# Optimization experiments

Hardware: AMD Instinct MI355X
Metric: run time of the kernel (lower is better)

Reference implementation:

```python
import jax, jax.numpy as jnp
import numpy as np

R = 128            # dense leaf-grid resolution (stand-in for N^3 octree leaves)
N_STEPS = 192      # fixed marching budget (replaces data-dependent while loop)
STEP_SIZE = 0.001
BACKGROUND = 1.0
DELTA_SCALE = 1.0  # 1/invradius with tree radius 1


def setup_inputs() -> dict:
    key = jax.random.key(0)
    k1, k2, k3, k4 = jax.random.split(key, 4)
    B = 65536
    grid = jax.random.normal(k1, (R, R, R, 4), dtype=jnp.float32)
    origins = jax.random.uniform(k2, (B, 3), dtype=jnp.float32)          # inside unit cube
    dirs = jax.random.normal(k3, (B, 3), dtype=jnp.float32)
    viewdirs = jax.random.normal(k4, (B, 3), dtype=jnp.float32)
    return {"grid": grid, "origins": origins, "dirs": dirs, "viewdirs": viewdirs}


def _dda_unit(cen, invdir):
    # entry/exit of ray cen + t*dir vs the unit cube [0,1]^3
    t1 = -cen * invdir            # [B,3]
    t2 = t1 + invdir
    lo = jnp.minimum(t1, t2)
    hi = jnp.maximum(t1, t2)
    tmin = jnp.maximum(jnp.max(lo, axis=-1), 0.0)   # [B]
    tmax = jnp.minimum(jnp.min(hi, axis=-1), 1e9)   # [B]
    return tmin, tmax


def _render(grid, origins, dirs, viewdirs):
    del viewdirs  # RGBA data_format: no SH basis evaluation
    dirs = dirs / jnp.linalg.norm(dirs, axis=-1, keepdims=True)
    invdirs = 1.0 / (dirs + 1e-9)
    t, tmax = _dda_unit(origins, invdirs)
    B = origins.shape[0]
    light = jnp.ones((B,), dtype=origins.dtype)
    out_rgb = jnp.zeros((B, 3), dtype=origins.dtype)
    cube_sz = 1.0 / R

    def step(carry, _):
        t, light, out_rgb = carry
        active = t < tmax
        pos = origins + t[:, None] * dirs                      # [B,3]
        idxf = jnp.floor(pos * R)
        idx = jnp.clip(idxf.astype(jnp.int32), 0, R - 1)       # voxel index
        rgba = grid[idx[:, 0], idx[:, 1], idx[:, 2]]           # [B,4] gather
        pos_t = pos * R - idx.astype(pos.dtype)                # local coords in voxel
        smin, smax = _dda_unit(pos_t, invdirs)
        delta_t = (smax - smin) * cube_sz + STEP_SIZE          # [B]
        sigma = jax.nn.relu(rgba[:, 3])
        att = jnp.exp(-delta_t * sigma * DELTA_SCALE)
        weight = light * (1.0 - att)
        rgb = jax.nn.sigmoid(rgba[:, :3])
        out_rgb = out_rgb + jnp.where(active[:, None], weight[:, None] * rgb, 0.0)
        light = jnp.where(active, light * att, light)
        t = jnp.where(active, t + delta_t, t)
        return (t, light, out_rgb), None

    (t, light, out_rgb), _ = jax.lax.scan(step, (t, light, out_rgb), None, length=N_STEPS)
    return out_rgb + BACKGROUND * light[:, None]


def reference(grid, origins, dirs, viewdirs):
    return _render(grid, origins, dirs, viewdirs)
```

## Files before the change

### kernel.cpp

```cpp
#include <hip/hip_runtime.h>


constexpr int   R_DIM    = 128;
constexpr int   N_VOX    = R_DIM * R_DIM * R_DIM;
constexpr int   N_STEPS  = 192;
constexpr int   NSEG     = 4;
constexpr int   SEG_LEN  = N_STEPS / NSEG;
constexpr float STEP_SZ  = 0.001f;
constexpr float CUBE_SZ  = 1.0f / 128.0f;
constexpr int   PIPE     = 8;
constexpr float SIG_MAX  = 5.5f;

__device__ __forceinline__ float sigmoid_fast(float x) {
    return __builtin_amdgcn_rcpf(1.0f + __expf(-x));
}

__device__ __forceinline__ void geom_step(
    float tl, float tmax,
    float oxR, float oyR, float ozR, float dxR, float dyR, float dzR,
    float ix, float iy, float iz, float ipx, float ipy, float ipz,
    int& i0, int& i1, int& i2, float& d)
{
    float px = __fadd_rn(oxR, __fmul_rn(tl, dxR));
    float py = __fadd_rn(oyR, __fmul_rn(tl, dyR));
    float pz = __fadd_rn(ozR, __fmul_rn(tl, dzR));

    float c0 = fminf(fmaxf(floorf(px), 0.0f), 127.0f);
    float c1 = fminf(fmaxf(floorf(py), 0.0f), 127.0f);
    float c2 = fminf(fmaxf(floorf(pz), 0.0f), 127.0f);
    i0 = (int)c0;
    i1 = (int)c1;
    i2 = (int)c2;

    float t1x = __fmul_rn(__fsub_rn(c0, px), ix);
    float t1y = __fmul_rn(__fsub_rn(c1, py), iy);
    float t1z = __fmul_rn(__fsub_rn(c2, pz), iz);
    float hix = __fadd_rn(t1x, ipx);
    float hiy = __fadd_rn(t1y, ipy);
    float hiz = __fadd_rn(t1z, ipz);
    float smax = fminf(fminf(fminf(hix, hiy), hiz), 1e9f);

    d = __fadd_rn(__fmul_rn(smax, CUBE_SZ), STEP_SZ);
    d = (tl < tmax) ? d : 0.0f;
}

__device__ __forceinline__ void ray_setup(
    const float* __restrict__ origins, const float* __restrict__ dirs, int i,
    float& oxR, float& oyR, float& ozR, float& dxR, float& dyR, float& dzR,
    float& ix, float& iy, float& iz,
    float& ipx, float& ipy, float& ipz,
    float& tmin, float& tmax)
{
    float ox = origins[3 * i + 0];
    float oy = origins[3 * i + 1];
    float oz = origins[3 * i + 2];
    float dx = dirs[3 * i + 0];
    float dy = dirs[3 * i + 1];
    float dz = dirs[3 * i + 2];

    float n2 = __fadd_rn(__fadd_rn(__fmul_rn(dx, dx), __fmul_rn(dy, dy)),
                         __fmul_rn(dz, dz));
    float nrm = sqrtf(n2);
    dx = dx / nrm;
    dy = dy / nrm;
    dz = dz / nrm;

    ix = 1.0f / __fadd_rn(dx, 1e-9f);
    iy = 1.0f / __fadd_rn(dy, 1e-9f);
    iz = 1.0f / __fadd_rn(dz, 1e-9f);

    ipx = fmaxf(ix, 0.0f);
    ipy = fmaxf(iy, 0.0f);
    ipz = fmaxf(iz, 0.0f);

    float t1x = __fmul_rn(-ox, ix), t2x = __fadd_rn(t1x, ix);
    float t1y = __fmul_rn(-oy, iy), t2y = __fadd_rn(t1y, iy);
    float t1z = __fmul_rn(-oz, iz), t2z = __fadd_rn(t1z, iz);
    float lox = fminf(t1x, t2x), hix = fmaxf(t1x, t2x);
    float loy = fminf(t1y, t2y), hiy = fmaxf(t1y, t2y);
    float loz = fminf(t1z, t2z), hiz = fmaxf(t1z, t2z);
    tmin = fmaxf(fmaxf(fmaxf(lox, loy), loz), 0.0f);
    tmax = fminf(fminf(fminf(hix, hiy), hiz), 1e9f);

    oxR = __fmul_rn(ox, 128.0f);
    oyR = __fmul_rn(oy, 128.0f);
    ozR = __fmul_rn(oz, 128.0f);
    dxR = __fmul_rn(dx, 128.0f);
    dyR = __fmul_rn(dy, 128.0f);
    dzR = __fmul_rn(dz, 128.0f);
}

__device__ __forceinline__ unsigned pack_voxel(float4 v) {
    unsigned ur = (unsigned)__float2int_rn(sigmoid_fast(v.x) * 255.0f);
    unsigned ug = (unsigned)__float2int_rn(sigmoid_fast(v.y) * 255.0f);
    unsigned ub = (unsigned)__float2int_rn(sigmoid_fast(v.z) * 255.0f);
    unsigned us = (unsigned)__float2int_rn(
        fminf(fmaxf(v.w, 0.0f), SIG_MAX) * (255.0f / SIG_MAX));
    return ur | (ug << 8) | (ub << 16) | (us << 24);
}

__global__ __launch_bounds__(256) void cvt_brick(
    const float4* __restrict__ g, uint4* __restrict__ gq4)
{
    int tid = blockIdx.x * blockDim.x + threadIdx.x;
    if (tid >= N_VOX / 4) return;
    int zq = tid & 31;
    int y  = (tid >> 5) & 127;
    int x  = tid >> 12;

    int src = (x * R_DIM + y) * R_DIM + 4 * zq;
    float4 v0 = g[src + 0];
    float4 v1 = g[src + 1];
    float4 v2 = g[src + 2];
    float4 v3 = g[src + 3];

    uint4 o;
    o.x = pack_voxel(v0);
    o.y = pack_voxel(v1);
    o.z = pack_voxel(v2);
    o.w = pack_voxel(v3);

    int bid = ((x >> 2) << 10) | ((y >> 2) << 5) | zq;
    int dst = bid * 16 + (x & 3) * 4 + (y & 3);
    gq4[dst] = o;
}

__global__ __launch_bounds__(256) void volrend_seg(
    const unsigned int* __restrict__ gq,
    const float* __restrict__ origins,
    const float* __restrict__ dirs,
    float* __restrict__ out,
    int B)
{
    __shared__ float4 lds[64 * (NSEG - 1)];

    int lane = threadIdx.x & 63;
    int seg  = threadIdx.x >> 6;
    int i = blockIdx.x * 64 + lane;

    float oxR, oyR, ozR, dxR, dyR, dzR, ix, iy, iz, ipx, ipy, ipz, tmin, tmax;
    ray_setup(origins, dirs, i, oxR, oyR, ozR, dxR, dyR, dzR,
              ix, iy, iz, ipx, ipy, ipz, tmin, tmax);

    float t = tmin;

    int pre_chunks = seg * (SEG_LEN / PIPE);
    for (int c = 0; c < pre_chunks; ++c) {
        if (t >= tmax) break;
        #pragma unroll
        for (int p = 0; p < PIPE; ++p) {
            int i0, i1, i2; float d;
            geom_step(t, tmax, oxR, oyR, ozR, dxR, dyR, dzR,
                      ix, iy, iz, ipx, ipy, ipz, i0, i1, i2, d);
            t = __fadd_rn(t, d);
        }
    }

    float light = 1.0f;
    float ar = 0.0f, ag = 0.0f, ab = 0.0f;

    for (int chunk = 0; chunk < SEG_LEN / PIPE; ++chunk) {
        if (t >= tmax) break;

        unsigned int val[PIPE];
        float del[PIPE];
        float tl = t;

        #pragma unroll
        for (int p = 0; p < PIPE; ++p) {
            int i0, i1, i2; float d;
            geom_step(tl, tmax, oxR, oyR, ozR, dxR, dyR, dzR,
                      ix, iy, iz, ipx, ipy, ipz, i0, i1, i2, d);
            unsigned bid = ((unsigned)(i0 >> 2) << 10) |
                           ((unsigned)(i1 >> 2) << 5) |
                           (unsigned)(i2 >> 2);
            unsigned loc = ((unsigned)(i0 & 3) << 4) |
                           ((unsigned)(i1 & 3) << 2) |
                           (unsigned)(i2 & 3);
            val[p] = gq[(bid << 6) | loc];
            del[p] = d;
            tl = __fadd_rn(tl, d);
        }

        #pragma unroll
        for (int p = 0; p < PIPE; ++p) {
            unsigned int v = val[p];
            float r  = (float)(v & 255u);
            float gg = (float)((v >> 8) & 255u);
            float b  = (float)((v >> 16) & 255u);
            float sg = (float)(v >> 24);
            float att = __expf(del[p] * (-SIG_MAX / 255.0f) * sg);
            float w  = light * (1.0f - att);
            float ws = w * (1.0f / 255.0f);
            ar = fmaf(ws, r, ar);
            ag = fmaf(ws, gg, ag);
            ab = fmaf(ws, b, ab);
            light *= att;
        }

        t = tl;
    }

    if (seg > 0) {
        lds[(seg - 1) * 64 + lane] = make_float4(ar, ag, ab, light);
    }
    __syncthreads();
    if (seg == 0) {
        float4 s1 = lds[0 * 64 + lane];
        float4 s2 = lds[1 * 64 + lane];
        float4 s3 = lds[2 * 64 + lane];
        float r3 = s3.x + s3.w, g3 = s3.y + s3.w, b3 = s3.z + s3.w;
        float r2 = fmaf(s2.w, r3, s2.x);
        float g2 = fmaf(s2.w, g3, s2.y);
        float b2 = fmaf(s2.w, b3, s2.z);
        float r1 = fmaf(s1.w, r2, s1.x);
        float g1 = fmaf(s1.w, g2, s1.y);
        float b1 = fmaf(s1.w, b2, s1.z);
        out[3 * i + 0] = fmaf(light, r1, ar);
        out[3 * i + 1] = fmaf(light, g1, ag);
        out[3 * i + 2] = fmaf(light, b1, ab);
    }
}

__global__ __launch_bounds__(256) void volrend_f32(
    const float* __restrict__ grid,
    const float* __restrict__ origins,
    const float* __restrict__ dirs,
    float* __restrict__ out,
    int B)
{
    int i = blockIdx.x * blockDim.x + threadIdx.x;
    if (i >= B) return;

    float oxR, oyR, ozR, dxR, dyR, dzR, ix, iy, iz, ipx, ipy, ipz, tmin, tmax;
    ray_setup(origins, dirs, i, oxR, oyR, ozR, dxR, dyR, dzR,
              ix, iy, iz, ipx, ipy, ipz, tmin, tmax);

    const float4* __restrict__ g4 = (const float4*)grid;

    float t = tmin;
    float light = 1.0f;
    float ar = 0.0f, ag = 0.0f, ab = 0.0f;

    for (int chunk = 0; chunk < N_STEPS / PIPE; ++chunk) {
        if (t >= tmax) break;

        float4 val[PIPE];
        float del[PIPE];
        float tl = t;

        #pragma unroll
        for (int p = 0; p < PIPE; ++p) {
            int i0, i1, i2; float d;
            geom_step(tl, tmax, oxR, oyR, ozR, dxR, dyR, dzR,
                      ix, iy, iz, ipx, ipy, ipz, i0, i1, i2, d);
            val[p] = g4[(i0 * R_DIM + i1) * R_DIM + i2];
            del[p] = d;
            tl = __fadd_rn(tl, d);
        }

        #pragma unroll
        for (int p = 0; p < PIPE; ++p) {
            float sigma = fmaxf(val[p].w, 0.0f);
            float att = __expf(-del[p] * sigma);
            float w = light * (1.0f - att);
            ar = fmaf(w, sigmoid_fast(val[p].x), ar);
            ag = fmaf(w, sigmoid_fast(val[p].y), ag);
            ab = fmaf(w, sigmoid_fast(val[p].z), ab);
            light *= att;
        }

        t = tl;
    }

    out[3 * i + 0] = ar + light;
    out[3 * i + 1] = ag + light;
    out[3 * i + 2] = ab + light;
}

extern "C" void kernel_launch(void* const* d_in, const int* in_sizes, int n_in,
                              void* d_out, int out_size, void* d_ws, size_t ws_size,
                              hipStream_t stream) {
    const float* grid    = (const float*)d_in[0];
    const float* origins = (const float*)d_in[1];
    const float* dirs    = (const float*)d_in[2];
    float* out = (float*)d_out;

    int B = in_sizes[1] / 3;

    size_t need = (size_t)N_VOX * 4;
    if (ws_size >= need && (B % 64) == 0) {
        uint4* gq4 = (uint4*)d_ws;
        cvt_brick<<<(N_VOX / 4 + 255) / 256, 256, 0, stream>>>(
            (const float4*)grid, gq4);
        volrend_seg<<<B / 64, 64 * NSEG, 0, stream>>>(
            (const unsigned int*)gq4, origins, dirs, out, B);
    } else {
        volrend_f32<<<(B + 255) / 256, 256, 0, stream>>>(grid, origins, dirs,
                                                         out, B);
    }
}
```

Baseline: 107.7 us.

## Precompute segment start checkpoints in fused prep kernel alongside grid conversion

Moves the per-segment geometry pre-walk out of the render kernel into a prep kernel that also does the brick conversion. Extra blocks walk each ray once and store the start t for segments 1..3 in workspace, so render waves for later segments no longer redo up to 144 geometry steps. This removes the redundant and imbalanced pre-walk work across the four segment waves. In exchange the walk becomes serial per ray in prep (one thread does all 144 steps), and it adds workspace traffic and a dependency between the two launches.

```diff
diff --git a/kernel.cpp b/kernel.cpp
--- a/kernel.cpp
+++ b/kernel.cpp
@@ -10,6 +10,7 @@
 constexpr float CUBE_SZ  = 1.0f / 128.0f;
 constexpr int   PIPE     = 8;
 constexpr float SIG_MAX  = 5.5f;
+constexpr int   CVT_BLOCKS = (N_VOX / 4 + 255) / 256;
 
 __device__ __forceinline__ float sigmoid_fast(float x) {
     return __builtin_amdgcn_rcpf(1.0f + __expf(-x));
@@ -99,10 +100,39 @@
     return ur | (ug << 8) | (ub << 16) | (us << 24);
 }
 
-__global__ __launch_bounds__(256) void cvt_brick(
-    const float4* __restrict__ g, uint4* __restrict__ gq4)
-{
-    int tid = blockIdx.x * blockDim.x + threadIdx.x;
+__global__ __launch_bounds__(256) void prep(
+    const float4* __restrict__ g, uint4* __restrict__ gq4,
+    const float* __restrict__ origins, const float* __restrict__ dirs,
+    float* __restrict__ cp, int B, int walk_blocks)
+{
+    if ((int)blockIdx.x < walk_blocks) {
+        int r = blockIdx.x * 256 + threadIdx.x;
+        if (r >= B) return;
+
+        float oxR, oyR, ozR, dxR, dyR, dzR, ix, iy, iz, ipx, ipy, ipz;
+        float tmin, tmax;
+        ray_setup(origins, dirs, r, oxR, oyR, ozR, dxR, dyR, dzR,
+                  ix, iy, iz, ipx, ipy, ipz, tmin, tmax);
+
+        float t = tmin;
+        #pragma unroll
+        for (int s = 1; s < NSEG; ++s) {
+            for (int c = 0; c < SEG_LEN / PIPE; ++c) {
+                if (t >= tmax) break;
+                #pragma unroll
+                for (int p = 0; p < PIPE; ++p) {
+                    int i0, i1, i2; float d;
+                    geom_step(t, tmax, oxR, oyR, ozR, dxR, dyR, dzR,
+                              ix, iy, iz, ipx, ipy, ipz, i0, i1, i2, d);
+                    t = __fadd_rn(t, d);
+                }
+            }
+            cp[(s - 1) * B + r] = t;
+        }
+        return;
+    }
+
+    int tid = (blockIdx.x - walk_blocks) * 256 + threadIdx.x;
     if (tid >= N_VOX / 4) return;
     int zq = tid & 31;
     int y  = (tid >> 5) & 127;
@@ -127,6 +157,7 @@
 
 __global__ __launch_bounds__(256) void volrend_seg(
     const unsigned int* __restrict__ gq,
+    const float* __restrict__ cp,
     const float* __restrict__ origins,
     const float* __restrict__ dirs,
     float* __restrict__ out,
@@ -142,19 +173,7 @@
     ray_setup(origins, dirs, i, oxR, oyR, ozR, dxR, dyR, dzR,
               ix, iy, iz, ipx, ipy, ipz, tmin, tmax);
 
-    float t = tmin;
-
-    int pre_chunks = seg * (SEG_LEN / PIPE);
-    for (int c = 0; c < pre_chunks; ++c) {
-        if (t >= tmax) break;
-        #pragma unroll
-        for (int p = 0; p < PIPE; ++p) {
-            int i0, i1, i2; float d;
-            geom_step(t, tmax, oxR, oyR, ozR, dxR, dyR, dzR,
-                      ix, iy, iz, ipx, ipy, ipz, i0, i1, i2, d);
-            t = __fadd_rn(t, d);
-        }
-    }
+    float t = (seg == 0) ? tmin : cp[(seg - 1) * B + i];
 
     float light = 1.0f;
     float ar = 0.0f, ag = 0.0f, ab = 0.0f;
@@ -288,13 +307,15 @@
 
     int B = in_sizes[1] / 3;
 
-    size_t need = (size_t)N_VOX * 4;
+    size_t need = (size_t)N_VOX * 4 + (size_t)3 * B * 4;
     if (ws_size >= need && (B % 64) == 0) {
         uint4* gq4 = (uint4*)d_ws;
-        cvt_brick<<<(N_VOX / 4 + 255) / 256, 256, 0, stream>>>(
-            (const float4*)grid, gq4);
+        float* cp  = (float*)((char*)d_ws + (size_t)N_VOX * 4);
+        int walk_blocks = (B + 255) / 256;
+        prep<<<walk_blocks + CVT_BLOCKS, 256, 0, stream>>>(
+            (const float4*)grid, gq4, origins, dirs, cp, B, walk_blocks);
         volrend_seg<<<B / 64, 64 * NSEG, 0, stream>>>(
-            (const unsigned int*)gq4, origins, dirs, out, B);
+            (const unsigned int*)gq4, cp, origins, dirs, out, B);
     } else {
         volrend_f32<<<(B + 255) / 256, 256, 0, stream>>>(grid, origins, dirs,
                                                          out, B);
```

Result: slower. 109.9 us (+2.0%).
